# Optimization experiments

Measured on AMD Instinct MI355X. Metric: run time of the kernel, lower is better.

The kernel has to match this reference:

```python
import jax, jax.numpy as jnp
import numpy as np

ALPHA = 1.702
LIMIT = 7.0

B, E = 128, 4          # tokens, top_k experts per token
N_EXPERTS = 32
K = 512                # d_model
C = 1024               # 2 * d_ff, interleaved glu/linear channels


def setup_inputs() -> dict:
    key = jax.random.key(0)
    k1, k2, k3, k4 = jax.random.split(key, 4)
    normed_x = jax.random.normal(k1, (B, K), dtype=jnp.float32)
    expert_indices = jax.random.randint(k2, (B, E), 0, N_EXPERTS, dtype=jnp.int32)
    mlp1_weight = jax.random.normal(k3, (N_EXPERTS, C, K), dtype=jnp.float32) * 0.02
    mlp1_bias = jax.random.normal(k4, (N_EXPERTS, C), dtype=jnp.float32) * 0.02
    return {
        "normed_x": normed_x,
        "expert_indices": expert_indices,
        "mlp1_weight": mlp1_weight,
        "mlp1_bias": mlp1_bias,
    }


def reference(normed_x, expert_indices, mlp1_weight, mlp1_bias):
    # Gather per-token expert weights/biases: [B,E,C,K] and [B,E,C]
    w = mlp1_weight[expert_indices]
    b = mlp1_bias[expert_indices]
    # Per-token batched matmul: t[b,e,c] = sum_k w[b,e,c,k] * x[b,k]
    t = jnp.einsum('beck,bk->bec', w, normed_x) + b
    # Interleaved split into gated / linear halves
    x_glu = jnp.minimum(t[..., ::2], LIMIT)               # clamp max only
    x_linear = jnp.clip(t[..., 1::2], -LIMIT, LIMIT)      # clamp both sides
    out_glu = x_glu * jax.nn.sigmoid(ALPHA * x_glu)
    return out_glu * (x_linear + 1.0)                     # [B, E, C//2]
```

## Files before the change

### kernel.cpp

```cpp
#include <hip/hip_runtime.h>
#include <hip/hip_bf16.h>

#define B_TOK   128
#define E_TOP   4
#define NEXP    32
#define KDIM    512
#define CDIM    1024
#define PAIRS   (B_TOK * E_TOP)
#define HALF_C  (CDIM / 2)

#define ALPHA   1.702f
#define LIMIT   7.0f

typedef __attribute__((ext_vector_type(8))) short short8;
typedef __attribute__((ext_vector_type(4))) float f32x4;

__device__ __forceinline__ unsigned pk2(float a, float b) {
    union { __hip_bfloat16 h; unsigned short u; } ca, cb;
    ca.h = __float2bfloat16(a);
    cb.h = __float2bfloat16(b);
    return (unsigned)ca.u | ((unsigned)cb.u << 16);
}

__device__ __forceinline__ short8 cvt8(float4 lo, float4 hi) {
    union { unsigned u[4]; short8 s; } r;
    r.u[0] = pk2(lo.x, lo.y);
    r.u[1] = pk2(lo.z, lo.w);
    r.u[2] = pk2(hi.x, hi.y);
    r.u[3] = pk2(hi.z, hi.w);
    return r.s;
}

__device__ __forceinline__ float glu_act(float g, float l) {
    g = fminf(g, LIMIT);
    l = fminf(fmaxf(l, -LIMIT), LIMIT);
    const float sg = 1.0f / (1.0f + __expf(-ALPHA * g));
    return (g * sg) * (l + 1.0f);
}

#define LDF4(p, off) (*(const float4*)((p) + (off)))

__global__ __launch_bounds__(256, 4) void moe_mlp1_kernel(
    const float* __restrict__ x,
    const int* __restrict__ idx,
    const float* __restrict__ w,
    const float* __restrict__ bias,
    float* __restrict__ out)
{
    __shared__ char  xbl[32 * 1024];
    __shared__ float red[2][64][8];
    __shared__ unsigned short list[PAIRS];
    __shared__ int cnt;

    const int e     = blockIdx.y;
    const int cBase = blockIdx.x * 32;
    const int tid   = threadIdx.x;
    const int wv    = tid >> 6;
    const int lane  = tid & 63;
    const int kh    = wv >> 1;
    const int cs    = wv & 1;
    const int kg    = lane >> 4;
    const int c16   = lane & 15;
    const int tA    = lane & 15;

    if (tid == 0) cnt = 0;
    __syncthreads();
    #pragma unroll
    for (int r = 0; r < 2; ++r) {
        const int p = tid + r * 256;
        if (idx[p] == e) {
            const int pos = atomicAdd(&cnt, 1);
            list[pos] = (unsigned short)p;
        }
    }
    __syncthreads();
    const int T = cnt;

    const float* wp = w + ((size_t)e * CDIM + cBase + cs * 16 + c16) * KDIM
                        + kh * 256 + kg * 8;
    const float4 bv = *(const float4*)(bias + (size_t)e * CDIM + cBase
                                       + cs * 16 + kg * 4);
    const int cb = cBase + cs * 16 + kg * 4;

    for (int tb = 0; tb < T; tb += 32) {
        if (tb) __syncthreads();
        const int nT = min(32, T - tb);

        #pragma unroll
        for (int r = 0; r < 2; ++r) {
            const int u = tid + r * 256;
            const int t = u & 31;
            const int s = u >> 5;
            const int pr = (int)list[tb + ((t < nT) ? t : 0)];
            const float* xr = x + (size_t)(pr >> 2) * KDIM + s * 32;
            const float4 f0 = LDF4(xr, 0),  f1 = LDF4(xr, 4);
            const float4 f2 = LDF4(xr, 8),  f3 = LDF4(xr, 12);
            const float4 f4 = LDF4(xr, 16), f5 = LDF4(xr, 20);
            const float4 f6 = LDF4(xr, 24), f7 = LDF4(xr, 28);
            char* db = &xbl[(s * 2 + (t >> 4)) * 1024 + (t & 15) * 16];
            *(short8*)(db + 0 * 256) = cvt8(f0, f1);
            *(short8*)(db + 1 * 256) = cvt8(f2, f3);
            *(short8*)(db + 2 * 256) = cvt8(f4, f5);
            *(short8*)(db + 3 * 256) = cvt8(f6, f7);
        }

        const int pr0 = (tA < nT)      ? (int)list[tb + tA]      : -1;
        const int pr1 = (tA + 16 < nT) ? (int)list[tb + tA + 16] : -1;

        __syncthreads();

        float4 w0[8], w1[8];
        #pragma unroll
        for (int p = 0; p < 8; ++p) {
            w0[p] = LDF4(wp, p * 32);
            w1[p] = LDF4(wp, p * 32 + 4);
        }

        f32x4 acc0 = {0.f, 0.f, 0.f, 0.f};
        f32x4 acc1 = {0.f, 0.f, 0.f, 0.f};
        const char* xb = &xbl[(kh * 8) * 2048 + lane * 16];

        #pragma unroll
        for (int s = 0; s < 8; ++s) {
            const short8 a  = cvt8(w0[s], w1[s]);
            const short8 b0 = *(const short8*)(xb + s * 2048);
            const short8 b1 = *(const short8*)(xb + s * 2048 + 1024);
            acc0 = __builtin_amdgcn_mfma_f32_16x16x32_bf16(a, b0, acc0, 0, 0, 0);
            acc1 = __builtin_amdgcn_mfma_f32_16x16x32_bf16(a, b1, acc1, 0, 0, 0);
        }

        if (kh == 1) {
            #pragma unroll
            for (int i = 0; i < 4; ++i) {
                red[cs][lane][i]     = acc0[i];
                red[cs][lane][4 + i] = acc1[i];
            }
        }
        __syncthreads();
        if (kh == 0) {
            #pragma unroll
            for (int i = 0; i < 4; ++i) {
                acc0[i] += red[cs][lane][i];
                acc1[i] += red[cs][lane][4 + i];
            }
            if (pr0 >= 0) {
                float2 o;
                o.x = glu_act(acc0[0] + bv.x, acc0[1] + bv.y);
                o.y = glu_act(acc0[2] + bv.z, acc0[3] + bv.w);
                *(float2*)&out[(size_t)pr0 * HALF_C + (cb >> 1)] = o;
            }
            if (pr1 >= 0) {
                float2 o;
                o.x = glu_act(acc1[0] + bv.x, acc1[1] + bv.y);
                o.y = glu_act(acc1[2] + bv.z, acc1[3] + bv.w);
                *(float2*)&out[(size_t)pr1 * HALF_C + (cb >> 1)] = o;
            }
        }
    }
}

extern "C" void kernel_launch(void* const* d_in, const int* in_sizes, int n_in,
                              void* d_out, int out_size, void* d_ws, size_t ws_size,
                              hipStream_t stream) {
    const float* x    = (const float*)d_in[0];
    const int*   idx  = (const int*)d_in[1];
    const float* w    = (const float*)d_in[2];
    const float* bias = (const float*)d_in[3];
    float* out = (float*)d_out;

    dim3 grid(CDIM / 32, NEXP);
    moe_mlp1_kernel<<<grid, 256, 0, stream>>>(x, idx, w, bias, out);
}
```

Measured before the change: 20.67 us.

## Split K across four waves with async global-to-LDS weight loads and ballot routing

Each block now handles 16 output channels and the grid is doubled. The four waves split K four ways, each wave staging its own weight slice into LDS through global_load_lds so the load is issued before expert routing runs. Routing is rebuilt per wave from ballot and popcount instead of a shared atomic list, and blocks whose expert has no tokens exit early. This removes block-wide syncs in the staging phase and overlaps the weight fetch with index scanning, but it adds a three-way cross-wave reduction, uses more LDS per block and lowers the occupancy hint to 2.

```diff
diff --git a/kernel.cpp b/kernel.cpp
--- a/kernel.cpp
+++ b/kernel.cpp
@@ -1,14 +1,11 @@
 #include <hip/hip_runtime.h>
 #include <hip/hip_bf16.h>
 
-#define B_TOK   128
-#define E_TOP   4
 #define NEXP    32
 #define KDIM    512
 #define CDIM    1024
-#define PAIRS   (B_TOK * E_TOP)
-#define HALF_C  (CDIM / 2)
-
+#define PAIRS   512
+#define HALF_C  512
 #define ALPHA   1.702f
 #define LIMIT   7.0f
 
@@ -40,108 +37,119 @@
 
 #define LDF4(p, off) (*(const float4*)((p) + (off)))
 
-__global__ __launch_bounds__(256, 4) void moe_mlp1_kernel(
+__global__ __launch_bounds__(256, 2) void moe_mlp1_kernel(
     const float* __restrict__ x,
     const int* __restrict__ idx,
     const float* __restrict__ w,
     const float* __restrict__ bias,
     float* __restrict__ out)
 {
-    __shared__ char  xbl[32 * 1024];
-    __shared__ float red[2][64][8];
-    __shared__ unsigned short list[PAIRS];
-    __shared__ int cnt;
+    __shared__ __align__(16) float wlds[4][2048];
+    __shared__ __align__(16) char  xlds[4][8192];
+    __shared__ unsigned short wls[4][PAIRS];
+    __shared__ __align__(16) float red[3][64][8];
 
     const int e     = blockIdx.y;
-    const int cBase = blockIdx.x * 32;
+    const int cBase = blockIdx.x * 16;
     const int tid   = threadIdx.x;
     const int wv    = tid >> 6;
     const int lane  = tid & 63;
-    const int kh    = wv >> 1;
-    const int cs    = wv & 1;
     const int kg    = lane >> 4;
     const int c16   = lane & 15;
     const int tA    = lane & 15;
 
-    if (tid == 0) cnt = 0;
-    __syncthreads();
+    int iv[8];
     #pragma unroll
-    for (int r = 0; r < 2; ++r) {
-        const int p = tid + r * 256;
-        if (idx[p] == e) {
-            const int pos = atomicAdd(&cnt, 1);
-            list[pos] = (unsigned short)p;
-        }
+    for (int c = 0; c < 8; ++c) iv[c] = idx[c * 64 + lane];
+
+    const float* wbase = w + ((size_t)(e * CDIM + cBase + c16)) * KDIM + wv * 128;
+    #pragma unroll
+    for (int j = 0; j < 8; ++j) {
+        const int s = j >> 1;
+        const int q = (j & 1) * 4 + kg;
+        const float* src = wbase + s * 32 + q * 4;
+        __builtin_amdgcn_global_load_lds(
+            (const __attribute__((address_space(1))) void*)src,
+            (__attribute__((address_space(3))) void*)&wlds[wv][j * 256],
+            16, 0, 0);
     }
-    __syncthreads();
-    const int T = cnt;
 
-    const float* wp = w + ((size_t)e * CDIM + cBase + cs * 16 + c16) * KDIM
-                        + kh * 256 + kg * 8;
-    const float4 bv = *(const float4*)(bias + (size_t)e * CDIM + cBase
-                                       + cs * 16 + kg * 4);
-    const int cb = cBase + cs * 16 + kg * 4;
+    const unsigned long long lt = (1ull << lane) - 1;
+    int T = 0;
+    #pragma unroll
+    for (int c = 0; c < 8; ++c) {
+        const bool hit = (iv[c] == e);
+        const unsigned long long m = __ballot(hit);
+        if (hit) wls[wv][T + (int)__popcll(m & lt)] = (unsigned short)(c * 64 + lane);
+        T += (int)__popcll(m);
+    }
+    if (T == 0) {
+        asm volatile("s_waitcnt vmcnt(0)" ::: "memory");
+        return;
+    }
+
+    const float4 bv = *(const float4*)(bias + (size_t)e * CDIM + cBase + kg * 4);
+    const int cb = cBase + kg * 4;
 
     for (int tb = 0; tb < T; tb += 32) {
-        if (tb) __syncthreads();
         const int nT = min(32, T - tb);
 
         #pragma unroll
         for (int r = 0; r < 2; ++r) {
-            const int u = tid + r * 256;
-            const int t = u & 31;
-            const int s = u >> 5;
-            const int pr = (int)list[tb + ((t < nT) ? t : 0)];
-            const float* xr = x + (size_t)(pr >> 2) * KDIM + s * 32;
-            const float4 f0 = LDF4(xr, 0),  f1 = LDF4(xr, 4);
-            const float4 f2 = LDF4(xr, 8),  f3 = LDF4(xr, 12);
-            const float4 f4 = LDF4(xr, 16), f5 = LDF4(xr, 20);
-            const float4 f6 = LDF4(xr, 24), f7 = LDF4(xr, 28);
-            char* db = &xbl[(s * 2 + (t >> 4)) * 1024 + (t & 15) * 16];
-            *(short8*)(db + 0 * 256) = cvt8(f0, f1);
-            *(short8*)(db + 1 * 256) = cvt8(f2, f3);
-            *(short8*)(db + 2 * 256) = cvt8(f4, f5);
-            *(short8*)(db + 3 * 256) = cvt8(f6, f7);
+            const int t = lane & 31;
+            const int s = (lane >> 5) + r * 2;
+            if (t < nT) {
+                const int pr = (int)wls[wv][tb + t];
+                const float* xr = x + (size_t)(pr >> 2) * KDIM + wv * 128 + s * 32;
+                const float4 f0 = LDF4(xr, 0),  f1 = LDF4(xr, 4);
+                const float4 f2 = LDF4(xr, 8),  f3 = LDF4(xr, 12);
+                const float4 f4 = LDF4(xr, 16), f5 = LDF4(xr, 20);
+                const float4 f6 = LDF4(xr, 24), f7 = LDF4(xr, 28);
+                char* db = &xlds[wv][(s * 2 + (t >> 4)) * 1024 + (t & 15) * 16];
+                *(short8*)(db + 0)   = cvt8(f0, f1);
+                *(short8*)(db + 256) = cvt8(f2, f3);
+                *(short8*)(db + 512) = cvt8(f4, f5);
+                *(short8*)(db + 768) = cvt8(f6, f7);
+            }
         }
 
-        const int pr0 = (tA < nT)      ? (int)list[tb + tA]      : -1;
-        const int pr1 = (tA + 16 < nT) ? (int)list[tb + tA + 16] : -1;
+        const int pr0 = (tA < nT)      ? (int)wls[wv][tb + tA]      : -1;
+        const int pr1 = (tA + 16 < nT) ? (int)wls[wv][tb + tA + 16] : -1;
 
-        __syncthreads();
-
-        float4 w0[8], w1[8];
-        #pragma unroll
-        for (int p = 0; p < 8; ++p) {
-            w0[p] = LDF4(wp, p * 32);
-            w1[p] = LDF4(wp, p * 32 + 4);
-        }
+        asm volatile("s_waitcnt vmcnt(0)" ::: "memory");
+        __builtin_amdgcn_sched_barrier(0);
 
         f32x4 acc0 = {0.f, 0.f, 0.f, 0.f};
         f32x4 acc1 = {0.f, 0.f, 0.f, 0.f};
-        const char* xb = &xbl[(kh * 8) * 2048 + lane * 16];
-
+        const char* xw = (const char*)&xlds[wv][0] + lane * 16;
+        const char* ww = (const char*)&wlds[wv][0] + kg * 512 + c16 * 16;
         #pragma unroll
-        for (int s = 0; s < 8; ++s) {
-            const short8 a  = cvt8(w0[s], w1[s]);
-            const short8 b0 = *(const short8*)(xb + s * 2048);
-            const short8 b1 = *(const short8*)(xb + s * 2048 + 1024);
-            acc0 = __builtin_amdgcn_mfma_f32_16x16x32_bf16(a, b0, acc0, 0, 0, 0);
-            acc1 = __builtin_amdgcn_mfma_f32_16x16x32_bf16(a, b1, acc1, 0, 0, 0);
+        for (int s = 0; s < 4; ++s) {
+            const float4 a0 = *(const float4*)(ww + s * 2048);
+            const float4 a1 = *(const float4*)(ww + s * 2048 + 256);
+            const short8 A  = cvt8(a0, a1);
+            const short8 B0 = *(const short8*)(xw + s * 2048);
+            const short8 B1 = *(const short8*)(xw + s * 2048 + 1024);
+            acc0 = __builtin_amdgcn_mfma_f32_16x16x32_bf16(A, B0, acc0, 0, 0, 0);
+            acc1 = __builtin_amdgcn_mfma_f32_16x16x32_bf16(A, B1, acc1, 0, 0, 0);
         }
 
-        if (kh == 1) {
-            #pragma unroll
-            for (int i = 0; i < 4; ++i) {
-                red[cs][lane][i]     = acc0[i];
-                red[cs][lane][4 + i] = acc1[i];
-            }
+        __syncthreads();
+        if (wv != 0) {
+            float* rp = &red[wv - 1][lane][0];
+            *(f32x4*)rp       = acc0;
+            *(f32x4*)(rp + 4) = acc1;
         }
         __syncthreads();
-        if (kh == 0) {
+        if (wv == 0) {
             #pragma unroll
-            for (int i = 0; i < 4; ++i) {
-                acc0[i] += red[cs][lane][i];
-                acc1[i] += red[cs][lane][4 + i];
+            for (int rr = 0; rr < 3; ++rr) {
+                const float* rp = &red[rr][lane][0];
+                #pragma unroll
+                for (int i = 0; i < 4; ++i) {
+                    acc0[i] += rp[i];
+                    acc1[i] += rp[4 + i];
+                }
             }
             if (pr0 >= 0) {
                 float2 o;
@@ -168,6 +176,6 @@
     const float* bias = (const float*)d_in[3];
     float* out = (float*)d_out;
 
-    dim3 grid(CDIM / 32, NEXP);
+    dim3 grid(CDIM / 16, NEXP);
     moe_mlp1_kernel<<<grid, 256, 0, stream>>>(x, idx, w, bias, out);
 }
```

Result: slower. 28.18 us (+36.3%).
